# Optimization experiments

Hardware: AMD Instinct MI355X
Metric: run time of the kernel (lower is better)

Reference implementation:

```python
import jax, jax.numpy as jnp
import numpy as np

N_ENTITIES = 300000
N_ITEMS = 150000
N_USERS = 150000
N_EDGES = 2000000
N_INTER = 2000000
N_REL = 32
D = 64


def _scatter_mean(src, index, dim_size):
    # torch_scatter.scatter_mean: sum per segment divided by count; empty segments -> 0
    sums = jax.ops.segment_sum(src, index, num_segments=dim_size)
    cnt = jax.ops.segment_sum(jnp.ones((src.shape[0],), src.dtype), index, num_segments=dim_size)
    return sums / jnp.maximum(cnt, 1.0)[:, None]


def setup_inputs() -> dict:
    key = jax.random.key(0)
    ks = jax.random.split(key, 9)
    return {
        "entity_emb": jax.random.normal(ks[0], (N_ENTITIES, D), dtype=jnp.float32),
        "user_emb": jax.random.normal(ks[1], (N_USERS, D), dtype=jnp.float32),
        "edge_index": jax.random.randint(ks[2], (2, N_EDGES), 0, N_ENTITIES),
        "edge_type": jax.random.randint(ks[3], (N_EDGES,), 0, N_REL),
        "mat_row": jax.random.randint(ks[4], (N_INTER,), 0, N_USERS),
        "mat_col": jax.random.randint(ks[5], (N_INTER,), 0, N_ITEMS),
        "weight": jax.random.normal(ks[6], (N_REL, D), dtype=jnp.float32),
        "gate1_w": jax.random.normal(ks[7], (D, D), dtype=jnp.float32) * 0.1,
        "gate2_w": jax.random.normal(ks[8], (D, D), dtype=jnp.float32) * 0.1,
    }


def reference(entity_emb, user_emb, edge_index, edge_type, mat_row, mat_col, weight, gate1_w, gate2_w):
    head, tail = edge_index[0], edge_index[1]
    # KG aggregation: gather tail embeddings, modulate by relation emb, scatter-mean to head
    neigh_relation_emb = entity_emb[tail] * weight[edge_type]          # [E, D]
    entity_kg_agg = _scatter_mean(neigh_relation_emb, head, N_ENTITIES)
    item_kg_agg = entity_kg_agg[:N_ITEMS]                              # [I, D]
    att_kg_agg = entity_kg_agg[N_ITEMS:]                               # [Ent-I, D]
    # interaction aggregation: gather user emb by row, scatter-mean to item (col)
    item_int_agg = _scatter_mean(user_emb[mat_row], mat_col, N_ITEMS)  # [I, D]
    # gated fusion (F.linear: x @ W.T)
    gi = jax.nn.sigmoid(item_kg_agg @ gate1_w.T + item_int_agg @ gate2_w.T)
    item_emb_fusion = gi * item_kg_agg + (1.0 - gi) * item_int_agg
    # sparse mm with all-ones values == segment sum of fused item embs over users
    user_agg = jax.ops.segment_sum(item_emb_fusion[mat_col], mat_row, num_segments=N_USERS)
    final_entity_agg = jnp.concatenate([item_emb_fusion, att_kg_agg], axis=0)
    return (final_entity_agg, user_agg, item_kg_agg, item_int_agg)
```

## Files before the change

kernel.cpp:

```cpp
#include <hip/hip_runtime.h>

#define N_ENTITIES 300000
#define N_ITEMS    150000
#define N_USERS    150000
#define N_EDGES    2000000
#define N_INTER    2000000
#define D          64
#define N_TOT      (N_ENTITIES + N_ITEMS + N_USERS)
#define NXCD       8

__device__ __forceinline__ int xcc_id() {
    int x;
    asm volatile("s_getreg_b32 %0, hwreg(HW_REG_XCC_ID)" : "=s"(x));
    return x & (NXCD - 1);
}

__global__ void hist_rank_kernel(const int* __restrict__ head,
                                 const int* __restrict__ mat_col,
                                 const int* __restrict__ mat_row,
                                 int* __restrict__ cnt_x,
                                 int* __restrict__ r_ent,
                                 int* __restrict__ r_item,
                                 int* __restrict__ r_user) {
    int e = blockIdx.x * 256 + threadIdx.x;
    if (e >= N_EDGES) return;
    int x = xcc_id();
    int* __restrict__ mycnt = cnt_x + x * N_TOT;
    int xt = x << 24;
    int h = head[e], c = mat_col[e], r = mat_row[e];
    int a0 = atomicAdd(&mycnt[h], 1);
    int a1 = atomicAdd(&mycnt[N_ENTITIES + c], 1);
    int a2 = atomicAdd(&mycnt[N_ENTITIES + N_ITEMS + r], 1);
    r_ent[e]  = a0 | xt;
    r_item[e] = a1 | xt;
    r_user[e] = a2 | xt;
}

__global__ void transpose_gates_kernel(const float* __restrict__ g1,
                                       const float* __restrict__ g2,
                                       float* __restrict__ g1t,
                                       float* __restrict__ g2t) {
    int i = blockIdx.x * 256 + threadIdx.x;
    if (i >= 64 * 64) return;
    int o = i >> 6, k = i & 63;
    g1t[k * 64 + o] = g1[i];
    g2t[k * 64 + o] = g2[i];
}

__global__ __launch_bounds__(256) void scan_partial(const int* __restrict__ cnt_x,
                                                    int* __restrict__ incl,
                                                    int* __restrict__ bsums,
                                                    int n) {
    __shared__ int lds[256];
    int t = threadIdx.x;
    int base = blockIdx.x * 1024 + t * 4;
    int v0 = 0, v1 = 0, v2 = 0, v3 = 0;
    #pragma unroll
    for (int x = 0; x < NXCD; ++x) {
        const int* __restrict__ c = cnt_x + x * N_TOT;
        if (base + 0 < n) v0 += c[base + 0];
        if (base + 1 < n) v1 += c[base + 1];
        if (base + 2 < n) v2 += c[base + 2];
        if (base + 3 < n) v3 += c[base + 3];
    }
    int s = v0 + v1 + v2 + v3;
    lds[t] = s;
    __syncthreads();
    for (int off = 1; off < 256; off <<= 1) {
        int x = (t >= off) ? lds[t - off] : 0;
        __syncthreads();
        lds[t] += x;
        __syncthreads();
    }
    int excl = lds[t] - s;
    if (base + 0 < n) incl[base + 0] = excl + v0;
    if (base + 1 < n) incl[base + 1] = excl + v0 + v1;
    if (base + 2 < n) incl[base + 2] = excl + v0 + v1 + v2;
    if (base + 3 < n) incl[base + 3] = excl + s;
    if (t == 255) bsums[blockIdx.x] = lds[255];
}

__global__ __launch_bounds__(1024) void scan_bsums(int* __restrict__ bsums, int nb) {
    __shared__ int lds[1024];
    int t = threadIdx.x;
    lds[t] = (t < nb) ? bsums[t] : 0;
    __syncthreads();
    for (int off = 1; off < 1024; off <<= 1) {
        int x = (t >= off) ? lds[t - off] : 0;
        __syncthreads();
        lds[t] += x;
        __syncthreads();
    }
    if (t < nb) bsums[t] = lds[t];
}

__global__ void scan_finalize(const int* __restrict__ incl,
                              const int* __restrict__ bsums,
                              const int* __restrict__ cnt_x,
                              int* __restrict__ off_ent,
                              int* __restrict__ off_item,
                              int* __restrict__ off_user,
                              uint2* __restrict__ prefx) {
    int i = blockIdx.x * 256 + threadIdx.x;
    if (i >= N_TOT) return;
    int b = i >> 10;
    int g = incl[i] + ((b > 0) ? bsums[b - 1] : 0);

    unsigned lo = 0, hi = 0;
    int tot = 0;
    #pragma unroll
    for (int x = 0; x < NXCD; ++x) {
        unsigned p = (unsigned)(tot & 0xFF);
        if (x < 4) lo |= p << (8 * x);
        else       hi |= p << (8 * (x - 4));
        tot += cnt_x[x * N_TOT + i];
    }
    prefx[i] = make_uint2(lo, hi);

    if (i < N_ENTITIES) {
        off_ent[i + 1] = g;
        if (i == 0) { off_ent[0] = 0; }
    } else if (i < N_ENTITIES + N_ITEMS) {
        off_item[i - N_ENTITIES + 1] = g - N_EDGES;
        if (i == N_ENTITIES) { off_item[0] = 0; }
    } else {
        off_user[i - N_ENTITIES - N_ITEMS + 1] = g - 2 * N_EDGES;
        if (i == N_ENTITIES + N_ITEMS) { off_user[0] = 0; }
    }
}

__device__ __forceinline__ int pfx_get(uint2 p, int x) {
    return (int)(((x < 4) ? (p.x >> (8 * x)) : (p.y >> (8 * (x - 4)))) & 0xFFu);
}

__global__ void scatter_all_kernel(const int* __restrict__ head,
                                   const int* __restrict__ tail,
                                   const int* __restrict__ type,
                                   const int* __restrict__ mat_row,
                                   const int* __restrict__ mat_col,
                                   const int* __restrict__ r_ent,
                                   const int* __restrict__ r_item,
                                   const int* __restrict__ r_user,
                                   const int* __restrict__ off_ent,
                                   const int* __restrict__ off_item,
                                   const int* __restrict__ off_user,
                                   const uint2* __restrict__ prefx,
                                   int* __restrict__ tt_sorted,
                                   int* __restrict__ row_sorted,
                                   int* __restrict__ col_sorted) {
    int e = blockIdx.x * 256 + threadIdx.x;
    if (e >= N_EDGES) return;
    int h = head[e], t = tail[e], ty = type[e];
    int r = mat_row[e], c = mat_col[e];

    int v0 = r_ent[e];
    int v1 = r_item[e];
    int v2 = r_user[e];
    int p0 = pfx_get(prefx[h], v0 >> 24);
    int p1 = pfx_get(prefx[N_ENTITIES + c], v1 >> 24);
    int p2 = pfx_get(prefx[N_ENTITIES + N_ITEMS + r], v2 >> 24);

    tt_sorted[off_ent[h]  + p0 + (v0 & 0xFFFFFF)] = t | (ty << 19);
    row_sorted[off_item[c] + p1 + (v1 & 0xFFFFFF)] = r;
    col_sorted[off_user[r] + p2 + (v2 & 0xFFFFFF)] = c;
}

__global__ __launch_bounds__(256, 8) void agg_ent_kernel(
        const float* __restrict__ entity_emb, const float* __restrict__ weight,
        const int* __restrict__ off, const int* __restrict__ tt_sorted,
        float* __restrict__ out_item_kg, float* __restrict__ out_final) {
    int wave = threadIdx.x >> 6, lane = threadIdx.x & 63;
    int g = lane >> 4, q = lane & 15;
    int ent = blockIdx.x * 4 + wave;
    if (ent >= N_ENTITIES) return;
    int s = off[ent], e = off[ent + 1];
    int cnt = e - s;
    const float4* __restrict__ emb4 = (const float4*)entity_emb;
    const float4* __restrict__ wt4  = (const float4*)weight;
    float ax = 0.f, ay = 0.f, az = 0.f, aw = 0.f;
    for (int idx = s + g; idx < e; idx += 8) {
        int v0 = tt_sorted[idx];
        int i2 = idx + 4;
        bool p2 = (i2 < e);
        int v1 = p2 ? tt_sorted[i2] : 0;
        {
            int t = v0 & 0x7FFFF, w = v0 >> 19;
            float4 a = emb4[t * 16 + q];
            float4 b = wt4[w * 16 + q];
            ax += a.x * b.x; ay += a.y * b.y; az += a.z * b.z; aw += a.w * b.w;
        }
        if (p2) {
            int t = v1 & 0x7FFFF, w = v1 >> 19;
            float4 a = emb4[t * 16 + q];
            float4 b = wt4[w * 16 + q];
            ax += a.x * b.x; ay += a.y * b.y; az += a.z * b.z; aw += a.w * b.w;
        }
    }
    ax += __shfl_xor(ax, 16); ax += __shfl_xor(ax, 32);
    ay += __shfl_xor(ay, 16); ay += __shfl_xor(ay, 32);
    az += __shfl_xor(az, 16); az += __shfl_xor(az, 32);
    aw += __shfl_xor(aw, 16); aw += __shfl_xor(aw, 32);
    if (g == 0) {
        float inv = 1.0f / (float)(cnt > 1 ? cnt : 1);
        float4 r; r.x = ax * inv; r.y = ay * inv; r.z = az * inv; r.w = aw * inv;
        if (ent < N_ITEMS) ((float4*)out_item_kg)[ent * 16 + q] = r;
        else               ((float4*)out_final)[ent * 16 + q]   = r;
    }
}

__global__ __launch_bounds__(512, 6) void agg_item_fuse_kernel(
        const float* __restrict__ user_emb,
        const int* __restrict__ off, const int* __restrict__ row_sorted,
        const float* __restrict__ item_kg,
        const float* __restrict__ g1t, const float* __restrict__ g2t,
        float* __restrict__ out_item_int, float* __restrict__ out_final) {
    __shared__ float s_g1t[4096];
    __shared__ float s_g2t[4096];
    __shared__ float s_ii[8 * 64];

    {
        const float4* a = (const float4*)g1t;
        const float4* b = (const float4*)g2t;
        float4* sa = (float4*)s_g1t;
        float4* sb = (float4*)s_g2t;
        #pragma unroll
        for (int i = threadIdx.x; i < 1024; i += 512) { sa[i] = a[i]; sb[i] = b[i]; }
    }

    int wave = threadIdx.x >> 6, lane = threadIdx.x & 63;
    int g = lane >> 4, q = lane & 15;
    int item = blockIdx.x * 8 + wave;
    int s = off[item], e = off[item + 1];
    int cnt = e - s;
    const float4* __restrict__ ue4 = (const float4*)user_emb;
    float ax = 0.f, ay = 0.f, az = 0.f, aw = 0.f;
    for (int idx = s + g; idx < e; idx += 8) {
        int r0 = row_sorted[idx];
        int i2 = idx + 4;
        bool p2 = (i2 < e);
        int r1 = p2 ? row_sorted[i2] : 0;
        {
            float4 v = ue4[r0 * 16 + q];
            ax += v.x; ay += v.y; az += v.z; aw += v.w;
        }
        if (p2) {
            float4 v = ue4[r1 * 16 + q];
            ax += v.x; ay += v.y; az += v.z; aw += v.w;
        }
    }
    ax += __shfl_xor(ax, 16); ax += __shfl_xor(ax, 32);
    ay += __shfl_xor(ay, 16); ay += __shfl_xor(ay, 32);
    az += __shfl_xor(az, 16); az += __shfl_xor(az, 32);
    aw += __shfl_xor(aw, 16); aw += __shfl_xor(aw, 32);
    float inv = 1.0f / (float)(cnt > 1 ? cnt : 1);
    ax *= inv; ay *= inv; az *= inv; aw *= inv;
    if (g == 0) {
        float4 t; t.x = ax; t.y = ay; t.z = az; t.w = aw;
        *(float4*)&s_ii[wave * 64 + 4 * q] = t;
    }
    __syncthreads();

    const float* __restrict__ kgrow = item_kg + (long long)item * 64;
    float gx = 0.f, gy = 0.f, gz = 0.f, gw = 0.f;
    #pragma unroll 4
    for (int i = 0; i < 16; ++i) {
        int k = 16 * g + i;
        float kk = kgrow[k];
        float ik = s_ii[wave * 64 + k];
        float4 w1 = *(const float4*)&s_g1t[k * 64 + 4 * q];
        float4 w2 = *(const float4*)&s_g2t[k * 64 + 4 * q];
        gx += kk * w1.x + ik * w2.x;
        gy += kk * w1.y + ik * w2.y;
        gz += kk * w1.z + ik * w2.z;
        gw += kk * w1.w + ik * w2.w;
    }
    gx += __shfl_xor(gx, 16); gx += __shfl_xor(gx, 32);
    gy += __shfl_xor(gy, 16); gy += __shfl_xor(gy, 32);
    gz += __shfl_xor(gz, 16); gz += __shfl_xor(gz, 32);
    gw += __shfl_xor(gw, 16); gw += __shfl_xor(gw, 32);

    if (g == 0) {
        float4 kg4 = *(const float4*)&kgrow[4 * q];
        float4 ii4; ii4.x = ax; ii4.y = ay; ii4.z = az; ii4.w = aw;
        float4 o;
        float s0 = 1.0f / (1.0f + __expf(-gx)); o.x = s0 * kg4.x + (1.0f - s0) * ii4.x;
        float s1 = 1.0f / (1.0f + __expf(-gy)); o.y = s1 * kg4.y + (1.0f - s1) * ii4.y;
        float s2 = 1.0f / (1.0f + __expf(-gz)); o.z = s2 * kg4.z + (1.0f - s2) * ii4.z;
        float s3 = 1.0f / (1.0f + __expf(-gw)); o.w = s3 * kg4.w + (1.0f - s3) * ii4.w;
        ((float4*)out_item_int)[item * 16 + q] = ii4;
        ((float4*)out_final)[item * 16 + q]    = o;
    }
}

__global__ __launch_bounds__(256, 8) void agg_user_kernel(
        const float* __restrict__ fusion,
        const int* __restrict__ off, const int* __restrict__ col_sorted,
        float* __restrict__ out_user) {
    int wave = threadIdx.x >> 6, lane = threadIdx.x & 63;
    int g = lane >> 4, q = lane & 15;
    int user = blockIdx.x * 4 + wave;
    if (user >= N_USERS) return;
    int s = off[user], e = off[user + 1];
    const float4* __restrict__ f4 = (const float4*)fusion;
    float ax = 0.f, ay = 0.f, az = 0.f, aw = 0.f;
    for (int idx = s + g; idx < e; idx += 8) {
        int c0 = col_sorted[idx];
        int i2 = idx + 4;
        bool p2 = (i2 < e);
        int c1 = p2 ? col_sorted[i2] : 0;
        {
            float4 v = f4[c0 * 16 + q];
            ax += v.x; ay += v.y; az += v.z; aw += v.w;
        }
        if (p2) {
            float4 v = f4[c1 * 16 + q];
            ax += v.x; ay += v.y; az += v.z; aw += v.w;
        }
    }
    ax += __shfl_xor(ax, 16); ax += __shfl_xor(ax, 32);
    ay += __shfl_xor(ay, 16); ay += __shfl_xor(ay, 32);
    az += __shfl_xor(az, 16); az += __shfl_xor(az, 32);
    aw += __shfl_xor(aw, 16); aw += __shfl_xor(aw, 32);
    if (g == 0) {
        float4 r; r.x = ax; r.y = ay; r.z = az; r.w = aw;
        ((float4*)out_user)[user * 16 + q] = r;
    }
}


extern "C" void kernel_launch(void* const* d_in, const int* in_sizes, int n_in,
                              void* d_out, int out_size, void* d_ws, size_t ws_size,
                              hipStream_t stream) {
    const float* entity_emb = (const float*)d_in[0];
    const float* user_emb   = (const float*)d_in[1];
    const int*   edge_index = (const int*)d_in[2];
    const int*   edge_type  = (const int*)d_in[3];
    const int*   mat_row    = (const int*)d_in[4];
    const int*   mat_col    = (const int*)d_in[5];
    const float* weight     = (const float*)d_in[6];
    const float* g1         = (const float*)d_in[7];
    const float* g2         = (const float*)d_in[8];

    const int* edge_head = edge_index;
    const int* edge_tail = edge_index + N_EDGES;

    float* out = (float*)d_out;
    float* out_final    = out;
    float* out_user     = out + (long long)N_ENTITIES * D;
    float* out_item_kg  = out_user + (long long)N_USERS * D;
    float* out_item_int = out_item_kg + (long long)N_ITEMS * D;

    int* w = (int*)d_ws;
    float* g1t_glob = (float*)w;  w += 64 * 64;
    float* g2t_glob = (float*)w;  w += 64 * 64;
    uint2* prefx    = (uint2*)w;  w += 2 * N_TOT;
    int* cnt_x     = w;  w += NXCD * N_TOT;
    int* off_ent   = w;  w += N_ENTITIES + 1;
    int* off_item  = w;  w += N_ITEMS + 1;
    int* off_user  = w;  w += N_USERS + 1;
    int* incl_tmp  = w;  w += N_TOT;
    int* bsums     = w;  w += 1024;
    int* r_ent     = w;  w += N_EDGES;
    int* r_item    = w;  w += N_INTER;
    int* r_user    = w;  w += N_INTER;
    int* tt_sorted = w;  w += N_EDGES;
    int* row_sorted= w;  w += N_INTER;
    int* col_sorted= w;  w += N_INTER;

    hipMemsetAsync(cnt_x, 0, (size_t)NXCD * N_TOT * sizeof(int), stream);

    const int EB = (N_EDGES + 255) / 256;

    transpose_gates_kernel<<<16, 256, 0, stream>>>(g1, g2, g1t_glob, g2t_glob);

    hist_rank_kernel<<<EB, 256, 0, stream>>>(edge_head, mat_col, mat_row,
                                             cnt_x, r_ent, r_item, r_user);

    {
        int nb = (N_TOT + 1023) / 1024;
        scan_partial<<<nb, 256, 0, stream>>>(cnt_x, incl_tmp, bsums, N_TOT);
        scan_bsums<<<1, 1024, 0, stream>>>(bsums, nb);
        scan_finalize<<<(N_TOT + 255) / 256, 256, 0, stream>>>(
            incl_tmp, bsums, cnt_x, off_ent, off_item, off_user, prefx);
    }

    scatter_all_kernel<<<EB, 256, 0, stream>>>(
        edge_head, edge_tail, edge_type, mat_row, mat_col,
        r_ent, r_item, r_user, off_ent, off_item, off_user, prefx,
        tt_sorted, row_sorted, col_sorted);

    agg_ent_kernel<<<N_ENTITIES / 4, 256, 0, stream>>>(
        entity_emb, weight, off_ent, tt_sorted, out_item_kg, out_final);
    agg_item_fuse_kernel<<<N_ITEMS / 8, 512, 0, stream>>>(
        user_emb, off_item, row_sorted, out_item_kg, g1t_glob, g2t_glob,
        out_item_int, out_final);
    agg_user_kernel<<<N_USERS / 4, 256, 0, stream>>>(
        out_final, off_user, col_sorted, out_user);
}
```

Baseline: 1.072 ms.

## Store per-XCD absolute bases in place of packed prefixes; use workgroup-scope atomics

The scan finalize step now overwrites the per-XCD count array with absolute per-XCD base offsets. The scatter kernel then needs one gather per edge instead of separate offset and packed-prefix reads. This removes the prefx buffer and the 8-bit prefix packing, which also drops the 255-count limit on per-XCD prefixes. Histogram atomics are relaxed to workgroup scope, relying on each XCD owning its own counter slice, which is a memory-model risk if blocks on the same XCD don't share the L2 coherence point.

```diff
diff --git a/kernel.cpp b/kernel.cpp
--- a/kernel.cpp
+++ b/kernel.cpp
@@ -28,9 +28,12 @@
     int* __restrict__ mycnt = cnt_x + x * N_TOT;
     int xt = x << 24;
     int h = head[e], c = mat_col[e], r = mat_row[e];
-    int a0 = atomicAdd(&mycnt[h], 1);
-    int a1 = atomicAdd(&mycnt[N_ENTITIES + c], 1);
-    int a2 = atomicAdd(&mycnt[N_ENTITIES + N_ITEMS + r], 1);
+    int a0 = __hip_atomic_fetch_add(&mycnt[h], 1,
+                                    __ATOMIC_RELAXED, __HIP_MEMORY_SCOPE_WORKGROUP);
+    int a1 = __hip_atomic_fetch_add(&mycnt[N_ENTITIES + c], 1,
+                                    __ATOMIC_RELAXED, __HIP_MEMORY_SCOPE_WORKGROUP);
+    int a2 = __hip_atomic_fetch_add(&mycnt[N_ENTITIES + N_ITEMS + r], 1,
+                                    __ATOMIC_RELAXED, __HIP_MEMORY_SCOPE_WORKGROUP);
     r_ent[e]  = a0 | xt;
     r_item[e] = a1 | xt;
     r_user[e] = a2 | xt;
@@ -96,26 +99,25 @@
 
 __global__ void scan_finalize(const int* __restrict__ incl,
                               const int* __restrict__ bsums,
-                              const int* __restrict__ cnt_x,
+                              int* __restrict__ cnt_x,
                               int* __restrict__ off_ent,
                               int* __restrict__ off_item,
-                              int* __restrict__ off_user,
-                              uint2* __restrict__ prefx) {
+                              int* __restrict__ off_user) {
     int i = blockIdx.x * 256 + threadIdx.x;
     if (i >= N_TOT) return;
     int b = i >> 10;
     int g = incl[i] + ((b > 0) ? bsums[b - 1] : 0);
 
-    unsigned lo = 0, hi = 0;
+    int c[NXCD];
     int tot = 0;
     #pragma unroll
-    for (int x = 0; x < NXCD; ++x) {
-        unsigned p = (unsigned)(tot & 0xFF);
-        if (x < 4) lo |= p << (8 * x);
-        else       hi |= p << (8 * (x - 4));
-        tot += cnt_x[x * N_TOT + i];
-    }
-    prefx[i] = make_uint2(lo, hi);
+    for (int x = 0; x < NXCD; ++x) { c[x] = cnt_x[x * N_TOT + i]; tot += c[x]; }
+
+    int region = (i < N_ENTITIES) ? 0
+               : (i < N_ENTITIES + N_ITEMS) ? N_EDGES : 2 * N_EDGES;
+    int base = g - tot - region;
+    #pragma unroll
+    for (int x = 0; x < NXCD; ++x) { cnt_x[x * N_TOT + i] = base; base += c[x]; }
 
     if (i < N_ENTITIES) {
         off_ent[i + 1] = g;
@@ -129,10 +131,6 @@
     }
 }
 
-__device__ __forceinline__ int pfx_get(uint2 p, int x) {
-    return (int)(((x < 4) ? (p.x >> (8 * x)) : (p.y >> (8 * (x - 4)))) & 0xFFu);
-}
-
 __global__ void scatter_all_kernel(const int* __restrict__ head,
                                    const int* __restrict__ tail,
                                    const int* __restrict__ type,
@@ -141,10 +139,7 @@
                                    const int* __restrict__ r_ent,
                                    const int* __restrict__ r_item,
                                    const int* __restrict__ r_user,
-                                   const int* __restrict__ off_ent,
-                                   const int* __restrict__ off_item,
-                                   const int* __restrict__ off_user,
-                                   const uint2* __restrict__ prefx,
+                                   const int* __restrict__ cnt_x,
                                    int* __restrict__ tt_sorted,
                                    int* __restrict__ row_sorted,
                                    int* __restrict__ col_sorted) {
@@ -152,17 +147,13 @@
     if (e >= N_EDGES) return;
     int h = head[e], t = tail[e], ty = type[e];
     int r = mat_row[e], c = mat_col[e];
-
-    int v0 = r_ent[e];
-    int v1 = r_item[e];
-    int v2 = r_user[e];
-    int p0 = pfx_get(prefx[h], v0 >> 24);
-    int p1 = pfx_get(prefx[N_ENTITIES + c], v1 >> 24);
-    int p2 = pfx_get(prefx[N_ENTITIES + N_ITEMS + r], v2 >> 24);
-
-    tt_sorted[off_ent[h]  + p0 + (v0 & 0xFFFFFF)] = t | (ty << 19);
-    row_sorted[off_item[c] + p1 + (v1 & 0xFFFFFF)] = r;
-    col_sorted[off_user[r] + p2 + (v2 & 0xFFFFFF)] = c;
+    int v0 = r_ent[e], v1 = r_item[e], v2 = r_user[e];
+    int p0 = cnt_x[(v0 >> 24) * N_TOT + h]                         + (v0 & 0xFFFFFF);
+    int p1 = cnt_x[(v1 >> 24) * N_TOT + N_ENTITIES + c]            + (v1 & 0xFFFFFF);
+    int p2 = cnt_x[(v2 >> 24) * N_TOT + N_ENTITIES + N_ITEMS + r]  + (v2 & 0xFFFFFF);
+    tt_sorted[p0]  = t | (ty << 19);
+    row_sorted[p1] = r;
+    col_sorted[p2] = c;
 }
 
 __global__ __launch_bounds__(256, 8) void agg_ent_kernel(
@@ -353,7 +344,6 @@
     int* w = (int*)d_ws;
     float* g1t_glob = (float*)w;  w += 64 * 64;
     float* g2t_glob = (float*)w;  w += 64 * 64;
-    uint2* prefx    = (uint2*)w;  w += 2 * N_TOT;
     int* cnt_x     = w;  w += NXCD * N_TOT;
     int* off_ent   = w;  w += N_ENTITIES + 1;
     int* off_item  = w;  w += N_ITEMS + 1;
@@ -381,12 +371,12 @@
         scan_partial<<<nb, 256, 0, stream>>>(cnt_x, incl_tmp, bsums, N_TOT);
         scan_bsums<<<1, 1024, 0, stream>>>(bsums, nb);
         scan_finalize<<<(N_TOT + 255) / 256, 256, 0, stream>>>(
-            incl_tmp, bsums, cnt_x, off_ent, off_item, off_user, prefx);
+            incl_tmp, bsums, cnt_x, off_ent, off_item, off_user);
     }
 
     scatter_all_kernel<<<EB, 256, 0, stream>>>(
         edge_head, edge_tail, edge_type, mat_row, mat_col,
-        r_ent, r_item, r_user, off_ent, off_item, off_user, prefx,
+        r_ent, r_item, r_user, cnt_x,
         tt_sorted, row_sorted, col_sorted);
 
     agg_ent_kernel<<<N_ENTITIES / 4, 256, 0, stream>>>(
```

Measured after the change: 1.049 ms. -2.2%, faster.
